# Optimization experiments

Hardware: AMD Instinct MI355X
Metric: run time of the kernel (lower is better)

The kernel has to match this reference:

```python
import jax, jax.numpy as jnp
import numpy as np

N_NODES = 100000
N_EDGES = 1600000
N_GRAPHS = 1024
D_NODE = 128
D_EDGE = 32
H1 = 64
H2 = 16


def _p(key, shape):
    return jax.random.normal(key, shape, dtype=jnp.float32) * 0.05


def setup_inputs() -> dict:
    key = jax.random.key(0)
    ks = jax.random.split(key, 24)
    x = jax.random.normal(ks[0], (N_NODES, D_NODE), dtype=jnp.float32)
    edge_index = jax.random.randint(ks[1], (2, N_EDGES), 0, N_NODES, dtype=jnp.int64)
    edge_attr = jax.random.normal(ks[2], (N_EDGES, D_EDGE), dtype=jnp.float32)
    batch = jnp.sort(jax.random.randint(ks[3], (N_NODES,), 0, N_GRAPHS, dtype=jnp.int64))
    # layer 1 (TransformerConv in=128, out=64, edge_dim=32, heads=1)
    Wq1, bq1 = _p(ks[4], (D_NODE, H1)), _p(ks[5], (H1,))
    Wk1, bk1 = _p(ks[6], (D_NODE, H1)), _p(ks[7], (H1,))
    Wv1, bv1 = _p(ks[8], (D_NODE, H1)), _p(ks[9], (H1,))
    We1 = _p(ks[10], (D_EDGE, H1))  # lin_edge has no bias in PyG
    Ws1, bs1 = _p(ks[11], (D_NODE, H1)), _p(ks[12], (H1,))  # skip / root weight
    # layer 2 (in=64, out=16)
    Wq2, bq2 = _p(ks[13], (H1, H2)), _p(ks[14], (H2,))
    Wk2, bk2 = _p(ks[15], (H1, H2)), _p(ks[16], (H2,))
    Wv2, bv2 = _p(ks[17], (H1, H2)), _p(ks[18], (H2,))
    We2 = _p(ks[19], (D_EDGE, H2))
    Ws2, bs2 = _p(ks[20], (H1, H2)), _p(ks[21], (H2,))
    # final fc
    Wf, bf = _p(ks[22], (H2, 1)), _p(ks[23], (1,))
    return dict(x=x, edge_attr=edge_attr,
                Wq1=Wq1, bq1=bq1, Wk1=Wk1, bk1=bk1, Wv1=Wv1, bv1=bv1, We1=We1, Ws1=Ws1, bs1=bs1,
                Wq2=Wq2, bq2=bq2, Wk2=Wk2, bk2=bk2, Wv2=Wv2, bv2=bv2, We2=We2, Ws2=Ws2, bs2=bs2,
                Wf=Wf, bf=bf, edge_index=edge_index, batch=batch)


def transformer_conv(x, edge_index, edge_attr, Wq, bq, Wk, bk, Wv, bv, We, Ws, bs):
    # PyG TransformerConv, heads=1, concat=True, root_weight=True
    n = x.shape[0]
    c = Wq.shape[1]
    src, dst = edge_index[0], edge_index[1]
    q = x @ Wq + bq                      # [N, C]
    k = x @ Wk + bk                      # [N, C]
    v = x @ Wv + bv                      # [N, C]
    e = edge_attr @ We                   # [E, C]
    ke = k[src] + e                      # [E, C]
    ve = v[src] + e                      # [E, C]
    score = jnp.sum(q[dst] * ke, axis=-1) / jnp.sqrt(jnp.float32(c))  # [E]
    # segment softmax over incoming edges of each dst node
    m = jax.ops.segment_max(score, dst, num_segments=n)
    a = jnp.exp(score - m[dst])
    den = jax.ops.segment_sum(a, dst, num_segments=n)
    alpha = a / (den[dst] + 1e-16)
    out = jax.ops.segment_sum(ve * alpha[:, None], dst, num_segments=n)  # [N, C]
    return out + x @ Ws + bs


def reference(x, edge_attr, Wq1, bq1, Wk1, bk1, Wv1, bv1, We1, Ws1, bs1,
              Wq2, bq2, Wk2, bk2, Wv2, bv2, We2, Ws2, bs2, Wf, bf,
              edge_index, batch):
    h = jax.nn.relu(transformer_conv(x, edge_index, edge_attr,
                                     Wq1, bq1, Wk1, bk1, Wv1, bv1, We1, Ws1, bs1))
    h = jax.nn.relu(transformer_conv(h, edge_index, edge_attr,
                                     Wq2, bq2, Wk2, bk2, Wv2, bv2, We2, Ws2, bs2))
    # global mean pool over graphs
    sums = jax.ops.segment_sum(h, batch, num_segments=N_GRAPHS)          # [G, 16]
    cnt = jax.ops.segment_sum(jnp.ones((h.shape[0],), h.dtype), batch, num_segments=N_GRAPHS)
    z = sums / jnp.maximum(cnt, 1.0)[:, None]
    return jax.nn.sigmoid(z @ Wf + bf)                                    # [G, 1]
```

## Files before the change

kernel.cpp:

```cpp
#include <hip/hip_runtime.h>
#include <hip/hip_bf16.h>
#include <hip/hip_fp16.h>
#include <math.h>

#define N_NODES 100000
#define N_EDGES 1600000
#define N_GRAPHS 1024
#define NB_SCAN ((N_NODES + 255) / 256)
#define NODES_PER_CHUNK 25000
#define CHUNK_EDGE_CAP 450000

typedef _Float16 f16x8 __attribute__((ext_vector_type(8)));
typedef float f32x4 __attribute__((ext_vector_type(4)));

static __device__ __forceinline__ float bf2f(ushort u) {
    return __uint_as_float(((unsigned)u) << 16);
}
static __device__ __forceinline__ ushort f2bf(float f) {
    unsigned x = __float_as_uint(f);
    return (ushort)((x + 0x7fffu + ((x >> 16) & 1u)) >> 16);
}

__global__ __launch_bounds__(256) void conv_x(const float* __restrict__ x,
                                              __half* __restrict__ xh) {
    int i = blockIdx.x * blockDim.x + threadIdx.x;
    const float4* src = (const float4*)x;
    float4 a = src[2 * i], b = src[2 * i + 1];
    __half2 h0 = __floats2half2_rn(a.x, a.y);
    __half2 h1 = __floats2half2_rn(a.z, a.w);
    __half2 h2 = __floats2half2_rn(b.x, b.y);
    __half2 h3 = __floats2half2_rn(b.z, b.w);
    uint4 o = make_uint4(*(uint*)&h0, *(uint*)&h1, *(uint*)&h2, *(uint*)&h3);
    ((uint4*)xh)[i] = o;
}

__global__ __launch_bounds__(256) void prepack_W(const float* __restrict__ Wq,
        const float* __restrict__ Wk, const float* __restrict__ Wv,
        const float* __restrict__ Ws, __half* __restrict__ Bpack) {
    int tid = blockIdx.x * 256 + threadIdx.x;
    if (tid >= 4 * 4 * 4 * 64) return;
    int lane = tid & 63, nt = (tid >> 6) & 3, kt = (tid >> 8) & 3, w = (tid >> 10) & 3;
    const float* W = (w == 0) ? Wq : (w == 1) ? Wk : (w == 2) ? Wv : Ws;
    int col = nt * 16 + (lane & 15);
    int kbase = kt * 32 + (lane >> 4) * 8;
    __half* dst = Bpack + (size_t)tid * 8;
#pragma unroll
    for (int j = 0; j < 8; ++j) dst[j] = __float2half(W[(kbase + j) * 64 + col]);
}

__global__ __launch_bounds__(256) void node_lin1_mfma(const __half* __restrict__ xh,
        const float* __restrict__ bq, const float* __restrict__ bk,
        const float* __restrict__ bv, const float* __restrict__ bs,
        const __half* __restrict__ Bpack,
        float* __restrict__ q, uint* __restrict__ kvt, float* __restrict__ s) {
    __shared__ _Float16 As[64][136];
    int tid = threadIdx.x;
    int nb = blockIdx.x * 64;
    {
        int row = tid >> 2, seg = tid & 3;
        int nn = nb + row;
        uint4* dst = (uint4*)&As[row][seg * 32];
        if (nn < N_NODES) {
            const uint4* sp = (const uint4*)(xh + (size_t)nn * 128 + seg * 32);
            dst[0] = sp[0]; dst[1] = sp[1]; dst[2] = sp[2]; dst[3] = sp[3];
        } else {
            uint4 z = make_uint4(0, 0, 0, 0);
            dst[0] = z; dst[1] = z; dst[2] = z; dst[3] = z;
        }
    }
    __syncthreads();
    int wv = tid >> 6, lane = tid & 63;
    const f16x8* Bp = (const f16x8*)Bpack;
    f16x8 Bf[4][4];
#pragma unroll
    for (int kt = 0; kt < 4; ++kt)
#pragma unroll
        for (int nt = 0; nt < 4; ++nt)
            Bf[kt][nt] = Bp[((wv * 4 + kt) * 4 + nt) * 64 + lane];
    f32x4 acc[4][4];
#pragma unroll
    for (int mt = 0; mt < 4; ++mt)
#pragma unroll
        for (int nt = 0; nt < 4; ++nt) acc[mt][nt] = (f32x4){0.f, 0.f, 0.f, 0.f};
    int arow = lane & 15, akoff = (lane >> 4) * 8;
#pragma unroll
    for (int kt = 0; kt < 4; ++kt) {
        f16x8 a[4];
#pragma unroll
        for (int mt = 0; mt < 4; ++mt)
            a[mt] = *(const f16x8*)&As[mt * 16 + arow][kt * 32 + akoff];
#pragma unroll
        for (int mt = 0; mt < 4; ++mt)
#pragma unroll
            for (int nt = 0; nt < 4; ++nt)
                acc[mt][nt] = __builtin_amdgcn_mfma_f32_16x16x32_f16(
                    a[mt], Bf[kt][nt], acc[mt][nt], 0, 0, 0);
    }
    const float* bvec = (wv == 0) ? bq : (wv == 1) ? bk : (wv == 2) ? bv : bs;
    int colw = lane & 15;
    int rgrp = (lane >> 4) * 4;
#pragma unroll
    for (int nt = 0; nt < 4; ++nt) {
        float bias = bvec[nt * 16 + colw];
        int col = nt * 16 + colw;
#pragma unroll
        for (int mt = 0; mt < 4; ++mt) {
#pragma unroll
            for (int r = 0; r < 4; ++r) {
                int node = nb + mt * 16 + rgrp + r;
                if (node >= N_NODES) continue;
                float val = acc[mt][nt][r] + bias;
                if (wv == 0)      q[(size_t)node * 64 + col] = val;
                else if (wv == 1) ((ushort*)kvt)[((size_t)node * 64 + col) * 2]     = f2bf(val);
                else if (wv == 2) ((ushort*)kvt)[((size_t)node * 64 + col) * 2 + 1] = f2bf(val);
                else              s[(size_t)node * 64 + col] = val;
            }
        }
    }
}

__global__ __launch_bounds__(256) void node_lin2(const float* __restrict__ h,
                          const float* __restrict__ Wq, const float* __restrict__ bq,
                          const float* __restrict__ Wk, const float* __restrict__ bk,
                          const float* __restrict__ Wv, const float* __restrict__ bv,
                          const float* __restrict__ Ws, const float* __restrict__ bs,
                          float* __restrict__ q, uint* __restrict__ kvt,
                          float* __restrict__ s) {
    __shared__ float hs[32][65];
    int tid = threadIdx.x;
    int nb = blockIdx.x * 32;
    for (int i = tid; i < 32 * 64; i += 256) {
        int nn = nb + (i >> 6);
        hs[i >> 6][i & 63] = (nn < N_NODES) ? h[(size_t)nb * 64 + i] : 0.f;
    }
    __syncthreads();
    int w = tid >> 6, t = tid & 63, g = t >> 4, c = t & 15;
    const float* W = (w == 0) ? Wq : (w == 1) ? Wk : (w == 2) ? Wv : Ws;
    const float* b = (w == 0) ? bq : (w == 1) ? bk : (w == 2) ? bv : bs;
    float acc[8];
#pragma unroll
    for (int n = 0; n < 8; ++n) acc[n] = 0.f;
#pragma unroll 4
    for (int j = 0; j < 64; ++j) {
        float wv = W[j * 16 + c];
#pragma unroll
        for (int n = 0; n < 8; ++n) acc[n] += hs[g * 8 + n][j] * wv;
    }
    float bb = b[c];
#pragma unroll
    for (int n = 0; n < 8; ++n) {
        int nn = nb + g * 8 + n;
        if (nn >= N_NODES) break;
        float r = acc[n] + bb;
        if (w == 0)      q[(size_t)nn * 16 + c] = r;
        else if (w == 1) ((ushort*)kvt)[((size_t)nn * 16 + c) * 2]     = f2bf(r);
        else if (w == 2) ((ushort*)kvt)[((size_t)nn * 16 + c) * 2 + 1] = f2bf(r);
        else             s[(size_t)nn * 16 + c] = r;
    }
}

__global__ void hist_kernel(const int* __restrict__ ei, int* __restrict__ deg) {
    int e = blockIdx.x * blockDim.x + threadIdx.x;
    if (e < N_EDGES) atomicAdd(deg + ei[N_EDGES + e], 1);
}

__global__ __launch_bounds__(256) void scan_block(const int* __restrict__ deg,
        int* __restrict__ rowptr, int* __restrict__ bsum) {
    __shared__ int sd[256];
    int i = blockIdx.x * 256 + threadIdx.x;
    int v = (i < N_NODES) ? deg[i] : 0;
    sd[threadIdx.x] = v;
    __syncthreads();
    for (int off = 1; off < 256; off <<= 1) {
        int add = (threadIdx.x >= off) ? sd[threadIdx.x - off] : 0;
        __syncthreads();
        sd[threadIdx.x] += add;
        __syncthreads();
    }
    if (i < N_NODES) rowptr[i] = sd[threadIdx.x] - v;
    if (threadIdx.x == 255) bsum[blockIdx.x] = sd[255];
}

__global__ __launch_bounds__(512) void scan_bsum(int* __restrict__ bsum) {
    __shared__ int sd[512];
    int t = threadIdx.x;
    int v = (t < NB_SCAN) ? bsum[t] : 0;
    sd[t] = v;
    __syncthreads();
    for (int off = 1; off < 512; off <<= 1) {
        int add = (t >= off) ? sd[t - off] : 0;
        __syncthreads();
        sd[t] += add;
        __syncthreads();
    }
    if (t < NB_SCAN) bsum[t] = sd[t] - v;
}

__global__ void scan_add(int* __restrict__ rowptr, int* __restrict__ cursor,
                         const int* __restrict__ bsum) {
    int i = blockIdx.x * blockDim.x + threadIdx.x;
    if (i < N_NODES) {
        int r = rowptr[i] + bsum[i >> 8];
        rowptr[i] = r;
        cursor[i] = r;
    }
    if (i == 0) rowptr[N_NODES] = N_EDGES;
}

__global__ void scatter_kernel(const int* __restrict__ ei, int* __restrict__ cursor,
                               int2* __restrict__ sorted) {
    int e = blockIdx.x * blockDim.x + threadIdx.x;
    if (e >= N_EDGES) return;
    int d = ei[N_EDGES + e];
    int pos = atomicAdd(cursor + d, 1);
    sorted[pos] = make_int2(ei[e], e);
}

__global__ __launch_bounds__(256) void edge_mlp1(const int2* __restrict__ sorted,
        const int* __restrict__ rowptr, int n0, int n1,
        const float* __restrict__ ea, const float* __restrict__ We1,
        const float* __restrict__ We2,
        ushort* __restrict__ ep1, ushort* __restrict__ ep2) {
    __shared__ float ea_s[64][36];
    int pbeg = rowptr[n0], pend = rowptr[n1];
    int base = pbeg + blockIdx.x * 64;
    if (base >= pend) return;
    int nedges = pend - base; if (nedges > 64) nedges = 64;
    int tid = threadIdx.x;
    int e4 = tid >> 2, r = tid & 3;
    if (e4 < nedges) {
        int eid = sorted[base + e4].y;
        const float4* src = (const float4*)(ea + (size_t)eid * 32);
        ((float4*)ea_s[e4])[r * 2]     = src[r * 2];
        ((float4*)ea_s[e4])[r * 2 + 1] = src[r * 2 + 1];
    }
    __syncthreads();
    int w = tid >> 6, t = tid & 63;
    int c2 = t & 15, j0 = (t >> 4) * 8;
    float we[32];
#pragma unroll
    for (int j = 0; j < 32; ++j) we[j] = We1[j * 64 + t];
    float we2p[8];
#pragma unroll
    for (int i = 0; i < 8; ++i) we2p[i] = We2[(j0 + i) * 16 + c2];
    int e0 = w * 16;
    int ecnt = nedges - e0; if (ecnt > 16) ecnt = 16;
    for (int e = 0; e < ecnt; ++e) {
        const float4* row = (const float4*)ea_s[e0 + e];
        float et = 0.f;
#pragma unroll
        for (int r2 = 0; r2 < 8; ++r2) {
            float4 f = row[r2];
            et += f.x * we[4*r2] + f.y * we[4*r2+1] + f.z * we[4*r2+2] + f.w * we[4*r2+3];
        }
        ep1[(size_t)(base - pbeg + e0 + e) * 64 + t] = f2bf(et);
        const float* rowf = ea_s[e0 + e] + j0;
        float p2 = rowf[0] * we2p[0] + rowf[1] * we2p[1] + rowf[2] * we2p[2]
                 + rowf[3] * we2p[3] + rowf[4] * we2p[4] + rowf[5] * we2p[5]
                 + rowf[6] * we2p[6] + rowf[7] * we2p[7];
        p2 += __shfl_xor(p2, 16, 64);
        p2 += __shfl_xor(p2, 32, 64);
        if (t < 16) ep2[(size_t)(base + e0 + e) * 16 + t] = f2bf(p2);
    }
}

__global__ __launch_bounds__(256) void agg_l1(const int2* __restrict__ sorted,
        const int* __restrict__ rowptr, const ushort* __restrict__ ep1,
        const float* __restrict__ q, const uint* __restrict__ kvt,
        float* __restrict__ h, int n0, int n1) {
    int w = threadIdx.x >> 6, t = threadIdx.x & 63;
    int n = n0 + blockIdx.x * 4 + w;
    if (n >= n1) return;
    int g = t >> 4, c = t & 15;
    int pbeg = rowptr[n0];
    float4 q4 = ((const float4*)(q + (size_t)n * 64))[c];
    int beg = rowptr[n], end = rowptr[n + 1];
    float den = 0.f;
    float ax = 0.f, ay = 0.f, az = 0.f, aw = 0.f;
    int idx = beg + g;
    for (; idx + 4 < end; idx += 8) {
        int sA = sorted[idx].x, sB = sorted[idx + 4].x;
        uint4 kvA = ((const uint4*)(kvt + (size_t)sA * 64))[c];
        uint4 kvB = ((const uint4*)(kvt + (size_t)sB * 64))[c];
        ushort4 eA = ((const ushort4*)(ep1 + (size_t)(idx - pbeg) * 64))[c];
        ushort4 eB = ((const ushort4*)(ep1 + (size_t)(idx + 4 - pbeg) * 64))[c];
        float eA0 = bf2f(eA.x), eA1 = bf2f(eA.y), eA2 = bf2f(eA.z), eA3 = bf2f(eA.w);
        float eB0 = bf2f(eB.x), eB1 = bf2f(eB.y), eB2 = bf2f(eB.z), eB3 = bf2f(eB.w);
        float kA0 = bf2f((ushort)kvA.x), vA0 = bf2f((ushort)(kvA.x >> 16));
        float kA1 = bf2f((ushort)kvA.y), vA1 = bf2f((ushort)(kvA.y >> 16));
        float kA2 = bf2f((ushort)kvA.z), vA2 = bf2f((ushort)(kvA.z >> 16));
        float kA3 = bf2f((ushort)kvA.w), vA3 = bf2f((ushort)(kvA.w >> 16));
        float kB0 = bf2f((ushort)kvB.x), vB0 = bf2f((ushort)(kvB.x >> 16));
        float kB1 = bf2f((ushort)kvB.y), vB1 = bf2f((ushort)(kvB.y >> 16));
        float kB2 = bf2f((ushort)kvB.z), vB2 = bf2f((ushort)(kvB.z >> 16));
        float kB3 = bf2f((ushort)kvB.w), vB3 = bf2f((ushort)(kvB.w >> 16));
        float pA = q4.x * (kA0 + eA0) + q4.y * (kA1 + eA1)
                 + q4.z * (kA2 + eA2) + q4.w * (kA3 + eA3);
        float pB = q4.x * (kB0 + eB0) + q4.y * (kB1 + eB1)
                 + q4.z * (kB2 + eB2) + q4.w * (kB3 + eB3);
        pA += __shfl_xor(pA, 1, 64); pB += __shfl_xor(pB, 1, 64);
        pA += __shfl_xor(pA, 2, 64); pB += __shfl_xor(pB, 2, 64);
        pA += __shfl_xor(pA, 4, 64); pB += __shfl_xor(pB, 4, 64);
        pA += __shfl_xor(pA, 8, 64); pB += __shfl_xor(pB, 8, 64);
        float aA = __expf(pA * 0.125f), aB = __expf(pB * 0.125f);
        den += aA + aB;
        ax += aA * (vA0 + eA0) + aB * (vB0 + eB0);
        ay += aA * (vA1 + eA1) + aB * (vB1 + eB1);
        az += aA * (vA2 + eA2) + aB * (vB2 + eB2);
        aw += aA * (vA3 + eA3) + aB * (vB3 + eB3);
    }
    if (idx < end) {
        int s = sorted[idx].x;
        uint4 kv4 = ((const uint4*)(kvt + (size_t)s * 64))[c];
        ushort4 e4 = ((const ushort4*)(ep1 + (size_t)(idx - pbeg) * 64))[c];
        float e0 = bf2f(e4.x), e1 = bf2f(e4.y), e2 = bf2f(e4.z), e3 = bf2f(e4.w);
        float k0 = bf2f((ushort)kv4.x), v0 = bf2f((ushort)(kv4.x >> 16));
        float k1 = bf2f((ushort)kv4.y), v1 = bf2f((ushort)(kv4.y >> 16));
        float k2 = bf2f((ushort)kv4.z), v2 = bf2f((ushort)(kv4.z >> 16));
        float k3 = bf2f((ushort)kv4.w), v3 = bf2f((ushort)(kv4.w >> 16));
        float p = q4.x * (k0 + e0) + q4.y * (k1 + e1) + q4.z * (k2 + e2) + q4.w * (k3 + e3);
        p += __shfl_xor(p, 1, 64);
        p += __shfl_xor(p, 2, 64);
        p += __shfl_xor(p, 4, 64);
        p += __shfl_xor(p, 8, 64);
        float a = __expf(p * 0.125f);
        den += a;
        ax += a * (v0 + e0); ay += a * (v1 + e1);
        az += a * (v2 + e2); aw += a * (v3 + e3);
    }
    den += __shfl_xor(den, 16, 64); den += __shfl_xor(den, 32, 64);
    ax += __shfl_xor(ax, 16, 64);   ax += __shfl_xor(ax, 32, 64);
    ay += __shfl_xor(ay, 16, 64);   ay += __shfl_xor(ay, 32, 64);
    az += __shfl_xor(az, 16, 64);   az += __shfl_xor(az, 32, 64);
    aw += __shfl_xor(aw, 16, 64);   aw += __shfl_xor(aw, 32, 64);
    if (g == 0) {
        float4* hp = (float4*)(h + (size_t)n * 64) + c;
        float4 hv = *hp;
        float d = den + 1e-16f;
        float4 o;
        o.x = ax / d + hv.x; o.x = o.x > 0.f ? o.x : 0.f;
        o.y = ay / d + hv.y; o.y = o.y > 0.f ? o.y : 0.f;
        o.z = az / d + hv.z; o.z = o.z > 0.f ? o.z : 0.f;
        o.w = aw / d + hv.w; o.w = o.w > 0.f ? o.w : 0.f;
        *hp = o;
    }
}

__global__ __launch_bounds__(256) void agg_l2(const int2* __restrict__ sorted,
        const int* __restrict__ rowptr, const ushort* __restrict__ ep2,
        const float* __restrict__ q, const uint* __restrict__ kvt,
        const float* __restrict__ skip, const int* __restrict__ batch,
        float* __restrict__ sums, float* __restrict__ cnt) {
    int w = threadIdx.x >> 6, t = threadIdx.x & 63;
    int n = blockIdx.x * 4 + w;
    if (n >= N_NODES) return;
    int g = t >> 4, c = t & 15;
    float qv = q[(size_t)n * 16 + c];
    int beg = rowptr[n], end = rowptr[n + 1];
    float den = 0.f, acc = 0.f;
    int idx = beg + g;
    for (; idx + 12 < end; idx += 16) {
        int sA = sorted[idx].x,      sB = sorted[idx + 4].x;
        int sC = sorted[idx + 8].x,  sD = sorted[idx + 12].x;
        uint kvA = kvt[(size_t)sA * 16 + c];
        uint kvB = kvt[(size_t)sB * 16 + c];
        uint kvC = kvt[(size_t)sC * 16 + c];
        uint kvD = kvt[(size_t)sD * 16 + c];
        float eA = bf2f(ep2[(size_t)idx * 16 + c]);
        float eB = bf2f(ep2[(size_t)(idx + 4) * 16 + c]);
        float eC = bf2f(ep2[(size_t)(idx + 8) * 16 + c]);
        float eD = bf2f(ep2[(size_t)(idx + 12) * 16 + c]);
        float pA = qv * (bf2f((ushort)kvA) + eA);
        float pB = qv * (bf2f((ushort)kvB) + eB);
        float pC = qv * (bf2f((ushort)kvC) + eC);
        float pD = qv * (bf2f((ushort)kvD) + eD);
        pA += __shfl_xor(pA, 8, 64); pB += __shfl_xor(pB, 8, 64);
        pC += __shfl_xor(pC, 8, 64); pD += __shfl_xor(pD, 8, 64);
        pA += __shfl_xor(pA, 4, 64); pB += __shfl_xor(pB, 4, 64);
        pC += __shfl_xor(pC, 4, 64); pD += __shfl_xor(pD, 4, 64);
        pA += __shfl_xor(pA, 2, 64); pB += __shfl_xor(pB, 2, 64);
        pC += __shfl_xor(pC, 2, 64); pD += __shfl_xor(pD, 2, 64);
        pA += __shfl_xor(pA, 1, 64); pB += __shfl_xor(pB, 1, 64);
        pC += __shfl_xor(pC, 1, 64); pD += __shfl_xor(pD, 1, 64);
        float aA = __expf(pA * 0.25f), aB = __expf(pB * 0.25f);
        float aC = __expf(pC * 0.25f), aD = __expf(pD * 0.25f);
        den += (aA + aB) + (aC + aD);
        acc += aA * (bf2f((ushort)(kvA >> 16)) + eA)
             + aB * (bf2f((ushort)(kvB >> 16)) + eB)
             + aC * (bf2f((ushort)(kvC >> 16)) + eC)
             + aD * (bf2f((ushort)(kvD >> 16)) + eD);
    }
    for (; idx + 4 < end; idx += 8) {
        int sA = sorted[idx].x, sB = sorted[idx + 4].x;
        uint kvA = kvt[(size_t)sA * 16 + c];
        uint kvB = kvt[(size_t)sB * 16 + c];
        float eA = bf2f(ep2[(size_t)idx * 16 + c]);
        float eB = bf2f(ep2[(size_t)(idx + 4) * 16 + c]);
        float pA = qv * (bf2f((ushort)kvA) + eA);
        float pB = qv * (bf2f((ushort)kvB) + eB);
        pA += __shfl_xor(pA, 8, 64); pB += __shfl_xor(pB, 8, 64);
        pA += __shfl_xor(pA, 4, 64); pB += __shfl_xor(pB, 4, 64);
        pA += __shfl_xor(pA, 2, 64); pB += __shfl_xor(pB, 2, 64);
        pA += __shfl_xor(pA, 1, 64); pB += __shfl_xor(pB, 1, 64);
        float aA = __expf(pA * 0.25f), aB = __expf(pB * 0.25f);
        den += aA + aB;
        acc += aA * (bf2f((ushort)(kvA >> 16)) + eA)
             + aB * (bf2f((ushort)(kvB >> 16)) + eB);
    }
    if (idx < end) {
        int s = sorted[idx].x;
        uint kvp = kvt[(size_t)s * 16 + c];
        float e2 = bf2f(ep2[(size_t)idx * 16 + c]);
        float p = qv * (bf2f((ushort)kvp) + e2);
        p += __shfl_xor(p, 8, 64);
        p += __shfl_xor(p, 4, 64);
        p += __shfl_xor(p, 2, 64);
        p += __shfl_xor(p, 1, 64);
        float a = __expf(p * 0.25f);
        den += a;
        acc += a * (bf2f((ushort)(kvp >> 16)) + e2);
    }
    den += __shfl_xor(den, 16, 64);
    den += __shfl_xor(den, 32, 64);
    acc += __shfl_xor(acc, 16, 64);
    acc += __shfl_xor(acc, 32, 64);
    if (t < 16) {
        float r2 = acc / (den + 1e-16f) + skip[(size_t)n * 16 + c];
        r2 = r2 > 0.f ? r2 : 0.f;
        int gb = batch[n];
        atomicAdd(sums + gb * 16 + c, r2);
        if (c == 0) atomicAdd(cnt + gb, 1.0f);
    }
}

__global__ void final_fc(const float* __restrict__ sums, const float* __restrict__ cnt,
                         const float* __restrict__ Wf, const float* __restrict__ bf,
                         float* __restrict__ out) {
    int g = blockIdx.x * blockDim.x + threadIdx.x;
    if (g >= N_GRAPHS) return;
    float cc = cnt[g];
    cc = cc > 1.f ? cc : 1.f;
    float acc = bf[0];
#pragma unroll
    for (int c = 0; c < 16; ++c) acc += (sums[g * 16 + c] / cc) * Wf[c];
    out[g] = 1.f / (1.f + expf(-acc));
}

extern "C" void kernel_launch(void* const* d_in, const int* in_sizes, int n_in,
                              void* d_out, int out_size, void* d_ws, size_t ws_size,
                              hipStream_t stream) {
    const float* x    = (const float*)d_in[0];
    const float* ea   = (const float*)d_in[1];
    const float* Wq1  = (const float*)d_in[2];
    const float* bq1  = (const float*)d_in[3];
    const float* Wk1  = (const float*)d_in[4];
    const float* bk1  = (const float*)d_in[5];
    const float* Wv1  = (const float*)d_in[6];
    const float* bv1  = (const float*)d_in[7];
    const float* We1  = (const float*)d_in[8];
    const float* Ws1  = (const float*)d_in[9];
    const float* bs1  = (const float*)d_in[10];
    const float* Wq2  = (const float*)d_in[11];
    const float* bq2  = (const float*)d_in[12];
    const float* Wk2  = (const float*)d_in[13];
    const float* bk2  = (const float*)d_in[14];
    const float* Wv2  = (const float*)d_in[15];
    const float* bv2  = (const float*)d_in[16];
    const float* We2  = (const float*)d_in[17];
    const float* Ws2  = (const float*)d_in[18];
    const float* bs2  = (const float*)d_in[19];
    const float* Wf   = (const float*)d_in[20];
    const float* bf   = (const float*)d_in[21];
    const int*   ei   = (const int*)d_in[22];
    const int*   batch= (const int*)d_in[23];
    float* out = (float*)d_out;

    float* ws = (float*)d_ws;
    size_t off = 0;
    float* q1    = ws + off;          off += (size_t)N_NODES * 64;
    uint* kvt1   = (uint*)(ws + off); off += (size_t)N_NODES * 64;
    float* s1    = ws + off;          off += (size_t)N_NODES * 64;
    float* q2    = ws + off;          off += (size_t)N_NODES * 16;
    uint* kvt2   = (uint*)(ws + off); off += (size_t)N_NODES * 16;
    float* s2    = ws + off;          off += (size_t)N_NODES * 16;
    int2* sorted = (int2*)(ws + off); off += (size_t)N_EDGES * 2;
    ushort* ep1  = (ushort*)(ws + off); off += (size_t)CHUNK_EDGE_CAP * 32;
    ushort* ep2  = (ushort*)(ws + off); off += (size_t)N_EDGES * 8;
    int* rowptr  = (int*)(ws + off);  off += N_NODES + 2;
    int* cursor  = (int*)(ws + off);  off += N_NODES;
    int* bsum    = (int*)(ws + off);  off += 512;
    float* zerop = ws + off;
    int*   deg   = (int*)(ws + off);  off += N_NODES;
    float* sums  = ws + off;          off += (size_t)N_GRAPHS * 16;
    float* cnt   = ws + off;          off += N_GRAPHS;
    size_t zero_bytes = ((size_t)N_NODES + N_GRAPHS * 16 + N_GRAPHS) * sizeof(float);
    off = (off + 3) & ~(size_t)3;
    __half* Bpack = (__half*)(ws + off); off += 16384;
    __half* xh = (__half*)ep1;

    hipMemsetAsync(zerop, 0, zero_bytes, stream);

    conv_x<<<6250, 256, 0, stream>>>(x, xh);
    prepack_W<<<16, 256, 0, stream>>>(Wq1, Wk1, Wv1, Ws1, Bpack);

    hist_kernel<<<(N_EDGES + 255) / 256, 256, 0, stream>>>(ei, deg);
    scan_block<<<NB_SCAN, 256, 0, stream>>>(deg, rowptr, bsum);
    scan_bsum<<<1, 512, 0, stream>>>(bsum);
    scan_add<<<NB_SCAN, 256, 0, stream>>>(rowptr, cursor, bsum);
    scatter_kernel<<<(N_EDGES + 255) / 256, 256, 0, stream>>>(ei, cursor, sorted);

    node_lin1_mfma<<<(N_NODES + 63) / 64, 256, 0, stream>>>(xh, bq1, bk1, bv1, bs1,
                                                            Bpack, q1, kvt1, s1);

    int mlp_blocks = (CHUNK_EDGE_CAP + 63) / 64;
    for (int c = 0; c < 4; ++c) {
        int n0 = c * NODES_PER_CHUNK;
        int n1 = (c + 1) * NODES_PER_CHUNK;
        if (n1 > N_NODES) n1 = N_NODES;
        edge_mlp1<<<mlp_blocks, 256, 0, stream>>>(sorted, rowptr, n0, n1, ea,
                                                  We1, We2, ep1, ep2);
        agg_l1<<<(NODES_PER_CHUNK + 3) / 4, 256, 0, stream>>>(sorted, rowptr, ep1,
                                                              q1, kvt1, s1, n0, n1);
    }

    node_lin2<<<(N_NODES + 31) / 32, 256, 0, stream>>>(s1, Wq2, bq2, Wk2, bk2, Wv2, bv2,
                                                       Ws2, bs2, q2, kvt2, s2);
    agg_l2<<<(N_NODES + 3) / 4, 256, 0, stream>>>(sorted, rowptr, ep2, q2, kvt2,
                                                  s2, batch, sums, cnt);

    final_fc<<<(N_GRAPHS + 255) / 256, 256, 0, stream>>>(sums, cnt, Wf, bf, out);
}
```

Measured before the change: 782.3 us.

## Split sorted edge array into SoA and pre-gather layer-2 KV per chunk

Splits the interleaved (src, eid) sorted-edge array into two separate int arrays, so each consumer reads only the field it needs. Layer-2 aggregation now runs in three node chunks: a dedicated gather kernel first copies kvt2 rows into an edge-ordered buffer that reuses q1's storage, then agg_l2 reads that buffer contiguously instead of doing random per-edge gathers. This trades the random gathers inside agg_l2 for an extra write-and-read pass and more kernel launches. Edges beyond the fixed per-chunk capacity are silently dropped by the gather.

```diff
diff --git a/kernel.cpp b/kernel.cpp
--- a/kernel.cpp
+++ b/kernel.cpp
@@ -9,6 +9,8 @@
 #define NB_SCAN ((N_NODES + 255) / 256)
 #define NODES_PER_CHUNK 25000
 #define CHUNK_EDGE_CAP 450000
+#define AGG2_NODES_PER_CHUNK 33334
+#define AGG2_EDGE_CAP 800000
 
 typedef _Float16 f16x8 __attribute__((ext_vector_type(8)));
 typedef float f32x4 __attribute__((ext_vector_type(4)));
@@ -208,15 +210,16 @@
 }
 
 __global__ void scatter_kernel(const int* __restrict__ ei, int* __restrict__ cursor,
-                               int2* __restrict__ sorted) {
+                               int* __restrict__ srcs, int* __restrict__ eids) {
     int e = blockIdx.x * blockDim.x + threadIdx.x;
     if (e >= N_EDGES) return;
     int d = ei[N_EDGES + e];
     int pos = atomicAdd(cursor + d, 1);
-    sorted[pos] = make_int2(ei[e], e);
-}
-
-__global__ __launch_bounds__(256) void edge_mlp1(const int2* __restrict__ sorted,
+    srcs[pos] = ei[e];
+    eids[pos] = e;
+}
+
+__global__ __launch_bounds__(256) void edge_mlp1(const int* __restrict__ eids,
         const int* __restrict__ rowptr, int n0, int n1,
         const float* __restrict__ ea, const float* __restrict__ We1,
         const float* __restrict__ We2,
@@ -229,7 +232,7 @@
     int tid = threadIdx.x;
     int e4 = tid >> 2, r = tid & 3;
     if (e4 < nedges) {
-        int eid = sorted[base + e4].y;
+        int eid = eids[base + e4];
         const float4* src = (const float4*)(ea + (size_t)eid * 32);
         ((float4*)ea_s[e4])[r * 2]     = src[r * 2];
         ((float4*)ea_s[e4])[r * 2 + 1] = src[r * 2 + 1];
@@ -264,7 +267,7 @@
     }
 }
 
-__global__ __launch_bounds__(256) void agg_l1(const int2* __restrict__ sorted,
+__global__ __launch_bounds__(256) void agg_l1(const int* __restrict__ srcs,
         const int* __restrict__ rowptr, const ushort* __restrict__ ep1,
         const float* __restrict__ q, const uint* __restrict__ kvt,
         float* __restrict__ h, int n0, int n1) {
@@ -279,7 +282,7 @@
     float ax = 0.f, ay = 0.f, az = 0.f, aw = 0.f;
     int idx = beg + g;
     for (; idx + 4 < end; idx += 8) {
-        int sA = sorted[idx].x, sB = sorted[idx + 4].x;
+        int sA = srcs[idx], sB = srcs[idx + 4];
         uint4 kvA = ((const uint4*)(kvt + (size_t)sA * 64))[c];
         uint4 kvB = ((const uint4*)(kvt + (size_t)sB * 64))[c];
         ushort4 eA = ((const ushort4*)(ep1 + (size_t)(idx - pbeg) * 64))[c];
@@ -310,7 +313,7 @@
         aw += aA * (vA3 + eA3) + aB * (vB3 + eB3);
     }
     if (idx < end) {
-        int s = sorted[idx].x;
+        int s = srcs[idx];
         uint4 kv4 = ((const uint4*)(kvt + (size_t)s * 64))[c];
         ushort4 e4 = ((const ushort4*)(ep1 + (size_t)(idx - pbeg) * 64))[c];
         float e0 = bf2f(e4.x), e1 = bf2f(e4.y), e2 = bf2f(e4.z), e3 = bf2f(e4.w);
@@ -346,30 +349,44 @@
     }
 }
 
-__global__ __launch_bounds__(256) void agg_l2(const int2* __restrict__ sorted,
-        const int* __restrict__ rowptr, const ushort* __restrict__ ep2,
-        const float* __restrict__ q, const uint* __restrict__ kvt,
-        const float* __restrict__ skip, const int* __restrict__ batch,
-        float* __restrict__ sums, float* __restrict__ cnt) {
+__global__ __launch_bounds__(256) void gather_kv2(const int* __restrict__ srcs,
+        const int* __restrict__ rowptr, const uint* __restrict__ kvt2,
+        uint* __restrict__ kv2e, int n0, int n1) {
+    int pbeg = rowptr[n0], pend = rowptr[n1];
+    int nloc = pend - pbeg;
+    if (nloc > AGG2_EDGE_CAP) nloc = AGG2_EDGE_CAP;
+    int i = blockIdx.x * 256 + threadIdx.x;
+    if (i >= nloc * 16) return;
+    int e = i >> 4, c = i & 15;
+    kv2e[i] = kvt2[(size_t)srcs[pbeg + e] * 16 + c];
+}
+
+__global__ __launch_bounds__(256) void agg_l2(const int* __restrict__ rowptr,
+        const uint* __restrict__ kv2e, const ushort* __restrict__ ep2,
+        const float* __restrict__ q, const float* __restrict__ skip,
+        const int* __restrict__ batch, float* __restrict__ sums,
+        float* __restrict__ cnt, int n0, int n1) {
     int w = threadIdx.x >> 6, t = threadIdx.x & 63;
-    int n = blockIdx.x * 4 + w;
-    if (n >= N_NODES) return;
+    int n = n0 + blockIdx.x * 4 + w;
+    if (n >= n1) return;
     int g = t >> 4, c = t & 15;
+    int pbeg = rowptr[n0];
     float qv = q[(size_t)n * 16 + c];
     int beg = rowptr[n], end = rowptr[n + 1];
+    int deg = end - beg;
+    int nfull = deg & ~15;
     float den = 0.f, acc = 0.f;
-    int idx = beg + g;
-    for (; idx + 12 < end; idx += 16) {
-        int sA = sorted[idx].x,      sB = sorted[idx + 4].x;
-        int sC = sorted[idx + 8].x,  sD = sorted[idx + 12].x;
-        uint kvA = kvt[(size_t)sA * 16 + c];
-        uint kvB = kvt[(size_t)sB * 16 + c];
-        uint kvC = kvt[(size_t)sC * 16 + c];
-        uint kvD = kvt[(size_t)sD * 16 + c];
-        float eA = bf2f(ep2[(size_t)idx * 16 + c]);
-        float eB = bf2f(ep2[(size_t)(idx + 4) * 16 + c]);
-        float eC = bf2f(ep2[(size_t)(idx + 8) * 16 + c]);
-        float eD = bf2f(ep2[(size_t)(idx + 12) * 16 + c]);
+    for (int b = 0; b < nfull; b += 16) {
+        int e0 = beg + b + g * 4;
+        int l0 = e0 - pbeg;
+        uint kvA = kv2e[(size_t)l0 * 16 + c];
+        uint kvB = kv2e[(size_t)(l0 + 1) * 16 + c];
+        uint kvC = kv2e[(size_t)(l0 + 2) * 16 + c];
+        uint kvD = kv2e[(size_t)(l0 + 3) * 16 + c];
+        float eA = bf2f(ep2[(size_t)e0 * 16 + c]);
+        float eB = bf2f(ep2[(size_t)(e0 + 1) * 16 + c]);
+        float eC = bf2f(ep2[(size_t)(e0 + 2) * 16 + c]);
+        float eD = bf2f(ep2[(size_t)(e0 + 3) * 16 + c]);
         float pA = qv * (bf2f((ushort)kvA) + eA);
         float pB = qv * (bf2f((ushort)kvB) + eB);
         float pC = qv * (bf2f((ushort)kvC) + eC);
@@ -390,26 +407,8 @@
              + aC * (bf2f((ushort)(kvC >> 16)) + eC)
              + aD * (bf2f((ushort)(kvD >> 16)) + eD);
     }
-    for (; idx + 4 < end; idx += 8) {
-        int sA = sorted[idx].x, sB = sorted[idx + 4].x;
-        uint kvA = kvt[(size_t)sA * 16 + c];
-        uint kvB = kvt[(size_t)sB * 16 + c];
-        float eA = bf2f(ep2[(size_t)idx * 16 + c]);
-        float eB = bf2f(ep2[(size_t)(idx + 4) * 16 + c]);
-        float pA = qv * (bf2f((ushort)kvA) + eA);
-        float pB = qv * (bf2f((ushort)kvB) + eB);
-        pA += __shfl_xor(pA, 8, 64); pB += __shfl_xor(pB, 8, 64);
-        pA += __shfl_xor(pA, 4, 64); pB += __shfl_xor(pB, 4, 64);
-        pA += __shfl_xor(pA, 2, 64); pB += __shfl_xor(pB, 2, 64);
-        pA += __shfl_xor(pA, 1, 64); pB += __shfl_xor(pB, 1, 64);
-        float aA = __expf(pA * 0.25f), aB = __expf(pB * 0.25f);
-        den += aA + aB;
-        acc += aA * (bf2f((ushort)(kvA >> 16)) + eA)
-             + aB * (bf2f((ushort)(kvB >> 16)) + eB);
-    }
-    if (idx < end) {
-        int s = sorted[idx].x;
-        uint kvp = kvt[(size_t)s * 16 + c];
+    for (int idx = beg + nfull + g; idx < end; idx += 4) {
+        uint kvp = kv2e[(size_t)(idx - pbeg) * 16 + c];
         float e2 = bf2f(ep2[(size_t)idx * 16 + c]);
         float p = qv * (bf2f((ushort)kvp) + e2);
         p += __shfl_xor(p, 8, 64);
@@ -483,7 +482,8 @@
     float* q2    = ws + off;          off += (size_t)N_NODES * 16;
     uint* kvt2   = (uint*)(ws + off); off += (size_t)N_NODES * 16;
     float* s2    = ws + off;          off += (size_t)N_NODES * 16;
-    int2* sorted = (int2*)(ws + off); off += (size_t)N_EDGES * 2;
+    int* srcs    = (int*)(ws + off);  off += N_EDGES;
+    int* eids    = (int*)(ws + off);  off += N_EDGES;
     ushort* ep1  = (ushort*)(ws + off); off += (size_t)CHUNK_EDGE_CAP * 32;
     ushort* ep2  = (ushort*)(ws + off); off += (size_t)N_EDGES * 8;
     int* rowptr  = (int*)(ws + off);  off += N_NODES + 2;
@@ -497,6 +497,7 @@
     off = (off + 3) & ~(size_t)3;
     __half* Bpack = (__half*)(ws + off); off += 16384;
     __half* xh = (__half*)ep1;
+    uint* kv2e = (uint*)q1;
 
     hipMemsetAsync(zerop, 0, zero_bytes, stream);
 
@@ -507,7 +508,7 @@
     scan_block<<<NB_SCAN, 256, 0, stream>>>(deg, rowptr, bsum);
     scan_bsum<<<1, 512, 0, stream>>>(bsum);
     scan_add<<<NB_SCAN, 256, 0, stream>>>(rowptr, cursor, bsum);
-    scatter_kernel<<<(N_EDGES + 255) / 256, 256, 0, stream>>>(ei, cursor, sorted);
+    scatter_kernel<<<(N_EDGES + 255) / 256, 256, 0, stream>>>(ei, cursor, srcs, eids);
 
     node_lin1_mfma<<<(N_NODES + 63) / 64, 256, 0, stream>>>(xh, bq1, bk1, bv1, bs1,
                                                             Bpack, q1, kvt1, s1);
@@ -517,16 +518,24 @@
         int n0 = c * NODES_PER_CHUNK;
         int n1 = (c + 1) * NODES_PER_CHUNK;
         if (n1 > N_NODES) n1 = N_NODES;
-        edge_mlp1<<<mlp_blocks, 256, 0, stream>>>(sorted, rowptr, n0, n1, ea,
+        edge_mlp1<<<mlp_blocks, 256, 0, stream>>>(eids, rowptr, n0, n1, ea,
                                                   We1, We2, ep1, ep2);
-        agg_l1<<<(NODES_PER_CHUNK + 3) / 4, 256, 0, stream>>>(sorted, rowptr, ep1,
+        agg_l1<<<(NODES_PER_CHUNK + 3) / 4, 256, 0, stream>>>(srcs, rowptr, ep1,
                                                               q1, kvt1, s1, n0, n1);
     }
 
     node_lin2<<<(N_NODES + 31) / 32, 256, 0, stream>>>(s1, Wq2, bq2, Wk2, bk2, Wv2, bv2,
                                                        Ws2, bs2, q2, kvt2, s2);
-    agg_l2<<<(N_NODES + 3) / 4, 256, 0, stream>>>(sorted, rowptr, ep2, q2, kvt2,
-                                                  s2, batch, sums, cnt);
+
+    int gth_blocks = (AGG2_EDGE_CAP * 16 + 255) / 256;
+    for (int c = 0; c < 3; ++c) {
+        int n0 = c * AGG2_NODES_PER_CHUNK;
+        int n1 = (c + 1) * AGG2_NODES_PER_CHUNK;
+        if (n1 > N_NODES) n1 = N_NODES;
+        gather_kv2<<<gth_blocks, 256, 0, stream>>>(srcs, rowptr, kvt2, kv2e, n0, n1);
+        agg_l2<<<(AGG2_NODES_PER_CHUNK + 3) / 4, 256, 0, stream>>>(rowptr, kv2e, ep2,
+                                                q2, s2, batch, sums, cnt, n0, n1);
+    }
 
     final_fc<<<(N_GRAPHS + 255) / 256, 256, 0, stream>>>(sums, cnt, Wf, bf, out);
 }
```

Measured after the change: 946.4 us. 1.21x slower.

## Map one thread per node in layer-2 aggregation instead of one wavefront

Applied to the files above, without the earlier changes.

Layer-2 aggregation now gives each node a single thread instead of a 64-lane wavefront. Each thread loads the 16-channel q, kv and edge rows with vector loads and keeps all channel accumulators in registers, so the cross-lane shuffle reductions go away. The cost is uncoalesced per-thread gathers, imbalance from varying node degrees within a wavefront, higher register pressure, and about 17 atomics issued per thread to the graph sums.

```diff
diff --git a/kernel.cpp b/kernel.cpp
--- a/kernel.cpp
+++ b/kernel.cpp
@@ -351,86 +351,107 @@
         const float* __restrict__ q, const uint* __restrict__ kvt,
         const float* __restrict__ skip, const int* __restrict__ batch,
         float* __restrict__ sums, float* __restrict__ cnt) {
-    int w = threadIdx.x >> 6, t = threadIdx.x & 63;
-    int n = blockIdx.x * 4 + w;
+    int n = blockIdx.x * 256 + threadIdx.x;
     if (n >= N_NODES) return;
-    int g = t >> 4, c = t & 15;
-    float qv = q[(size_t)n * 16 + c];
+    float qr[16];
+    {
+        const float4* qp = (const float4*)(q + (size_t)n * 16);
+#pragma unroll
+        for (int i = 0; i < 4; ++i) {
+            float4 v = qp[i];
+            qr[4*i] = v.x; qr[4*i+1] = v.y; qr[4*i+2] = v.z; qr[4*i+3] = v.w;
+        }
+    }
+    float acc[16];
+#pragma unroll
+    for (int i = 0; i < 16; ++i) acc[i] = 0.f;
+    float den = 0.f;
     int beg = rowptr[n], end = rowptr[n + 1];
-    float den = 0.f, acc = 0.f;
-    int idx = beg + g;
-    for (; idx + 12 < end; idx += 16) {
-        int sA = sorted[idx].x,      sB = sorted[idx + 4].x;
-        int sC = sorted[idx + 8].x,  sD = sorted[idx + 12].x;
-        uint kvA = kvt[(size_t)sA * 16 + c];
-        uint kvB = kvt[(size_t)sB * 16 + c];
-        uint kvC = kvt[(size_t)sC * 16 + c];
-        uint kvD = kvt[(size_t)sD * 16 + c];
-        float eA = bf2f(ep2[(size_t)idx * 16 + c]);
-        float eB = bf2f(ep2[(size_t)(idx + 4) * 16 + c]);
-        float eC = bf2f(ep2[(size_t)(idx + 8) * 16 + c]);
-        float eD = bf2f(ep2[(size_t)(idx + 12) * 16 + c]);
-        float pA = qv * (bf2f((ushort)kvA) + eA);
-        float pB = qv * (bf2f((ushort)kvB) + eB);
-        float pC = qv * (bf2f((ushort)kvC) + eC);
-        float pD = qv * (bf2f((ushort)kvD) + eD);
-        pA += __shfl_xor(pA, 8, 64); pB += __shfl_xor(pB, 8, 64);
-        pC += __shfl_xor(pC, 8, 64); pD += __shfl_xor(pD, 8, 64);
-        pA += __shfl_xor(pA, 4, 64); pB += __shfl_xor(pB, 4, 64);
-        pC += __shfl_xor(pC, 4, 64); pD += __shfl_xor(pD, 4, 64);
-        pA += __shfl_xor(pA, 2, 64); pB += __shfl_xor(pB, 2, 64);
-        pC += __shfl_xor(pC, 2, 64); pD += __shfl_xor(pD, 2, 64);
-        pA += __shfl_xor(pA, 1, 64); pB += __shfl_xor(pB, 1, 64);
-        pC += __shfl_xor(pC, 1, 64); pD += __shfl_xor(pD, 1, 64);
-        float aA = __expf(pA * 0.25f), aB = __expf(pB * 0.25f);
-        float aC = __expf(pC * 0.25f), aD = __expf(pD * 0.25f);
-        den += (aA + aB) + (aC + aD);
-        acc += aA * (bf2f((ushort)(kvA >> 16)) + eA)
-             + aB * (bf2f((ushort)(kvB >> 16)) + eB)
-             + aC * (bf2f((ushort)(kvC >> 16)) + eC)
-             + aD * (bf2f((ushort)(kvD >> 16)) + eD);
-    }
-    for (; idx + 4 < end; idx += 8) {
-        int sA = sorted[idx].x, sB = sorted[idx + 4].x;
-        uint kvA = kvt[(size_t)sA * 16 + c];
-        uint kvB = kvt[(size_t)sB * 16 + c];
-        float eA = bf2f(ep2[(size_t)idx * 16 + c]);
-        float eB = bf2f(ep2[(size_t)(idx + 4) * 16 + c]);
-        float pA = qv * (bf2f((ushort)kvA) + eA);
-        float pB = qv * (bf2f((ushort)kvB) + eB);
-        pA += __shfl_xor(pA, 8, 64); pB += __shfl_xor(pB, 8, 64);
-        pA += __shfl_xor(pA, 4, 64); pB += __shfl_xor(pB, 4, 64);
-        pA += __shfl_xor(pA, 2, 64); pB += __shfl_xor(pB, 2, 64);
-        pA += __shfl_xor(pA, 1, 64); pB += __shfl_xor(pB, 1, 64);
+    int idx = beg;
+    for (; idx + 2 <= end; idx += 2) {
+        int sA = sorted[idx].x, sB = sorted[idx + 1].x;
+        const uint4* kpA = (const uint4*)(kvt + (size_t)sA * 16);
+        const uint4* kpB = (const uint4*)(kvt + (size_t)sB * 16);
+        uint4 kA0 = kpA[0], kA1 = kpA[1], kA2 = kpA[2], kA3 = kpA[3];
+        uint4 kB0 = kpB[0], kB1 = kpB[1], kB2 = kpB[2], kB3 = kpB[3];
+        const uint4* eppA = (const uint4*)(ep2 + (size_t)idx * 16);
+        uint4 eA0 = eppA[0], eA1 = eppA[1];
+        const uint4* eppB = (const uint4*)(ep2 + (size_t)(idx + 1) * 16);
+        uint4 eB0 = eppB[0], eB1 = eppB[1];
+        uint kwA[16], kwB[16], ewA[8], ewB[8];
+        kwA[0]=kA0.x; kwA[1]=kA0.y; kwA[2]=kA0.z; kwA[3]=kA0.w;
+        kwA[4]=kA1.x; kwA[5]=kA1.y; kwA[6]=kA1.z; kwA[7]=kA1.w;
+        kwA[8]=kA2.x; kwA[9]=kA2.y; kwA[10]=kA2.z; kwA[11]=kA2.w;
+        kwA[12]=kA3.x; kwA[13]=kA3.y; kwA[14]=kA3.z; kwA[15]=kA3.w;
+        kwB[0]=kB0.x; kwB[1]=kB0.y; kwB[2]=kB0.z; kwB[3]=kB0.w;
+        kwB[4]=kB1.x; kwB[5]=kB1.y; kwB[6]=kB1.z; kwB[7]=kB1.w;
+        kwB[8]=kB2.x; kwB[9]=kB2.y; kwB[10]=kB2.z; kwB[11]=kB2.w;
+        kwB[12]=kB3.x; kwB[13]=kB3.y; kwB[14]=kB3.z; kwB[15]=kB3.w;
+        ewA[0]=eA0.x; ewA[1]=eA0.y; ewA[2]=eA0.z; ewA[3]=eA0.w;
+        ewA[4]=eA1.x; ewA[5]=eA1.y; ewA[6]=eA1.z; ewA[7]=eA1.w;
+        ewB[0]=eB0.x; ewB[1]=eB0.y; ewB[2]=eB0.z; ewB[3]=eB0.w;
+        ewB[4]=eB1.x; ewB[5]=eB1.y; ewB[6]=eB1.z; ewB[7]=eB1.w;
+        float pA = 0.f, pB = 0.f;
+#pragma unroll
+        for (int c = 0; c < 16; ++c) {
+            float eAc = bf2f((ushort)(ewA[c >> 1] >> ((c & 1) * 16)));
+            float eBc = bf2f((ushort)(ewB[c >> 1] >> ((c & 1) * 16)));
+            pA += qr[c] * (bf2f((ushort)kwA[c]) + eAc);
+            pB += qr[c] * (bf2f((ushort)kwB[c]) + eBc);
+        }
         float aA = __expf(pA * 0.25f), aB = __expf(pB * 0.25f);
         den += aA + aB;
-        acc += aA * (bf2f((ushort)(kvA >> 16)) + eA)
-             + aB * (bf2f((ushort)(kvB >> 16)) + eB);
+#pragma unroll
+        for (int c = 0; c < 16; ++c) {
+            float eAc = bf2f((ushort)(ewA[c >> 1] >> ((c & 1) * 16)));
+            float eBc = bf2f((ushort)(ewB[c >> 1] >> ((c & 1) * 16)));
+            acc[c] += aA * (bf2f((ushort)(kwA[c] >> 16)) + eAc)
+                    + aB * (bf2f((ushort)(kwB[c] >> 16)) + eBc);
+        }
     }
     if (idx < end) {
-        int s = sorted[idx].x;
-        uint kvp = kvt[(size_t)s * 16 + c];
-        float e2 = bf2f(ep2[(size_t)idx * 16 + c]);
-        float p = qv * (bf2f((ushort)kvp) + e2);
-        p += __shfl_xor(p, 8, 64);
-        p += __shfl_xor(p, 4, 64);
-        p += __shfl_xor(p, 2, 64);
-        p += __shfl_xor(p, 1, 64);
-        float a = __expf(p * 0.25f);
-        den += a;
-        acc += a * (bf2f((ushort)(kvp >> 16)) + e2);
-    }
-    den += __shfl_xor(den, 16, 64);
-    den += __shfl_xor(den, 32, 64);
-    acc += __shfl_xor(acc, 16, 64);
-    acc += __shfl_xor(acc, 32, 64);
-    if (t < 16) {
-        float r2 = acc / (den + 1e-16f) + skip[(size_t)n * 16 + c];
-        r2 = r2 > 0.f ? r2 : 0.f;
-        int gb = batch[n];
-        atomicAdd(sums + gb * 16 + c, r2);
-        if (c == 0) atomicAdd(cnt + gb, 1.0f);
-    }
+        int sA = sorted[idx].x;
+        const uint4* kpA = (const uint4*)(kvt + (size_t)sA * 16);
+        uint4 kA0 = kpA[0], kA1 = kpA[1], kA2 = kpA[2], kA3 = kpA[3];
+        const uint4* eppA = (const uint4*)(ep2 + (size_t)idx * 16);
+        uint4 eA0 = eppA[0], eA1 = eppA[1];
+        uint kwA[16], ewA[8];
+        kwA[0]=kA0.x; kwA[1]=kA0.y; kwA[2]=kA0.z; kwA[3]=kA0.w;
+        kwA[4]=kA1.x; kwA[5]=kA1.y; kwA[6]=kA1.z; kwA[7]=kA1.w;
+        kwA[8]=kA2.x; kwA[9]=kA2.y; kwA[10]=kA2.z; kwA[11]=kA2.w;
+        kwA[12]=kA3.x; kwA[13]=kA3.y; kwA[14]=kA3.z; kwA[15]=kA3.w;
+        ewA[0]=eA0.x; ewA[1]=eA0.y; ewA[2]=eA0.z; ewA[3]=eA0.w;
+        ewA[4]=eA1.x; ewA[5]=eA1.y; ewA[6]=eA1.z; ewA[7]=eA1.w;
+        float pA = 0.f;
+#pragma unroll
+        for (int c = 0; c < 16; ++c) {
+            float eAc = bf2f((ushort)(ewA[c >> 1] >> ((c & 1) * 16)));
+            pA += qr[c] * (bf2f((ushort)kwA[c]) + eAc);
+        }
+        float aA = __expf(pA * 0.25f);
+        den += aA;
+#pragma unroll
+        for (int c = 0; c < 16; ++c) {
+            float eAc = bf2f((ushort)(ewA[c >> 1] >> ((c & 1) * 16)));
+            acc[c] += aA * (bf2f((ushort)(kwA[c] >> 16)) + eAc);
+        }
+    }
+    float d = den + 1e-16f;
+    const float4* sp = (const float4*)(skip + (size_t)n * 16);
+    int gb = batch[n];
+#pragma unroll
+    for (int i = 0; i < 4; ++i) {
+        float4 sv = sp[i];
+        float r0 = acc[4*i]     / d + sv.x; r0 = r0 > 0.f ? r0 : 0.f;
+        float r1 = acc[4*i + 1] / d + sv.y; r1 = r1 > 0.f ? r1 : 0.f;
+        float r2 = acc[4*i + 2] / d + sv.z; r2 = r2 > 0.f ? r2 : 0.f;
+        float r3 = acc[4*i + 3] / d + sv.w; r3 = r3 > 0.f ? r3 : 0.f;
+        atomicAdd(sums + gb * 16 + 4*i,     r0);
+        atomicAdd(sums + gb * 16 + 4*i + 1, r1);
+        atomicAdd(sums + gb * 16 + 4*i + 2, r2);
+        atomicAdd(sums + gb * 16 + 4*i + 3, r3);
+    }
+    atomicAdd(cnt + gb, 1.0f);
 }
 
 __global__ void final_fc(const float* __restrict__ sums, const float* __restrict__ cnt,
@@ -525,8 +546,8 @@
 
     node_lin2<<<(N_NODES + 31) / 32, 256, 0, stream>>>(s1, Wq2, bq2, Wk2, bk2, Wv2, bv2,
                                                        Ws2, bs2, q2, kvt2, s2);
-    agg_l2<<<(N_NODES + 3) / 4, 256, 0, stream>>>(sorted, rowptr, ep2, q2, kvt2,
-                                                  s2, batch, sums, cnt);
+    agg_l2<<<(N_NODES + 255) / 256, 256, 0, stream>>>(sorted, rowptr, ep2, q2, kvt2,
+                                                      s2, batch, sums, cnt);
 
     final_fc<<<(N_GRAPHS + 255) / 256, 256, 0, stream>>>(sums, cnt, Wf, bf, out);
 }
```

Result: slower. 860.8 us (+10.0%).
